# Optimization experiments

Hardware: AMD Instinct MI355X
Metric: run time of the kernel (lower is better)

## Reference

```python
import jax, jax.numpy as jnp
import numpy as np

HOP = 2
N = 16384
HIDDEN = 64


def setup_inputs() -> dict:
    key = jax.random.key(0)
    k1, k2, k3 = jax.random.split(key, 3)
    user_embs = jax.random.normal(k1, (N, HIDDEN), dtype=jnp.float32)
    adj = jax.random.uniform(k2, (N, N), dtype=jnp.float32)
    # xavier-uniform-like scale for [2*HIDDEN, HIDDEN] weights
    limit = float(np.sqrt(6.0 / (2 * HIDDEN + HIDDEN)))
    W = jax.random.uniform(k3, (HOP, 2 * HIDDEN, HIDDEN), dtype=jnp.float32,
                           minval=-limit, maxval=limit)
    return {"user_embs": user_embs, "adj": adj, "W": W}


def reference(user_embs, adj, W):
    # DiffNet social GCN: hop rounds of aggregate -> concat -> dense -> tanh.
    # Dropout omitted (eval mode, training=False).
    x = user_embs
    for k in range(HOP):
        agg = adj @ x                                  # [N, H] neighbor aggregation
        x = jnp.tanh(jnp.concatenate([agg, x], axis=1) @ W[k])  # [N, H]
    return x
```

## Files before the change

### kernel.cpp

```cpp
#include <hip/hip_runtime.h>
#include <hip/hip_bf16.h>
#include <math.h>

#define NROWS 16384
#define HID 64
#define KSPLIT 8
#define KCH (NROWS / KSPLIT)

typedef __attribute__((ext_vector_type(8))) __bf16 bf16x8;
typedef __attribute__((ext_vector_type(4))) float f32x4;

__device__ inline f32x4 mfma16(bf16x8 a, bf16x8 b, f32x4 c) {
    return __builtin_amdgcn_mfma_f32_16x16x32_bf16(a, b, c, 0, 0, 0);
}

__device__ inline void split8v(const f32x4 v0, const f32x4 v1, bf16x8& h, bf16x8& l) {
    float f[8] = {v0[0], v0[1], v0[2], v0[3], v1[0], v1[1], v1[2], v1[3]};
#pragma unroll
    for (int j = 0; j < 8; ++j) {
        __bf16 hh = (__bf16)f[j];
        h[j] = hh;
        l[j] = (__bf16)(f[j] - (float)hh);
    }
}

__global__ __launch_bounds__(256) void pack_b(const float* __restrict__ x,
                                              __bf16* __restrict__ hi,
                                              __bf16* __restrict__ lo) {
    __shared__ float tile[32 * 64];
    const int kb = blockIdx.x;
    const f32x4* src = (const f32x4*)(x + (size_t)kb * 32 * 64);
    f32x4* dst = (f32x4*)tile;
    dst[threadIdx.x] = src[threadIdx.x];
    dst[threadIdx.x + 256] = src[threadIdx.x + 256];
    __syncthreads();
    const int t = threadIdx.x >> 6;
    const int l = threadIdx.x & 63;
    const int col = (t << 4) + (l & 15);
    const int krow = (l >> 4) * 8;
    bf16x8 h8, l8;
#pragma unroll
    for (int j = 0; j < 8; ++j) {
        float v = tile[(krow + j) * 64 + col];
        __bf16 hh = (__bf16)v;
        h8[j] = hh;
        l8[j] = (__bf16)(v - (float)hh);
    }
    const size_t base = (((size_t)kb * 4 + t) * 64 + l) * 8;
    *(bf16x8*)(hi + base) = h8;
    *(bf16x8*)(lo + base) = l8;
}

__global__ __launch_bounds__(256, 2) void gemm_partial(const float* __restrict__ adj,
                                                       const __bf16* __restrict__ Bhi,
                                                       const __bf16* __restrict__ Blo,
                                                       float* __restrict__ partial) {
    const int lane = threadIdx.x & 63;
    const int wv = threadIdx.x >> 6;
    const int rt = blockIdx.x & 63;
    const int ks = blockIdx.x >> 6;
    const int rbase = rt * 256 + wv * 64;
    const int rq = lane & 15;
    const int kq = lane >> 4;

    f32x4 acc[4][4];
#pragma unroll
    for (int g = 0; g < 4; ++g)
#pragma unroll
        for (int t = 0; t < 4; ++t) acc[g][t] = f32x4{0.f, 0.f, 0.f, 0.f};

    const float* ap = adj + (size_t)(rbase + rq) * NROWS + ks * KCH + kq * 8;
    const int kk0 = ks * KCH;

    for (int kk = 0; kk < KCH; kk += 32) {
        f32x4 av[4][2];
#pragma unroll
        for (int g = 0; g < 4; ++g) {
            const f32x4* a = (const f32x4*)(ap + (size_t)(g * 16) * NROWS + kk);
            av[g][0] = a[0];
            av[g][1] = a[1];
        }
        const size_t bb = ((size_t)((kk0 + kk) >> 5) * 4) * 512 + (size_t)lane * 8;
        bf16x8 bh[4], bl[4];
#pragma unroll
        for (int t = 0; t < 4; ++t) {
            bh[t] = *(const bf16x8*)(Bhi + bb + (size_t)t * 512);
            bl[t] = *(const bf16x8*)(Blo + bb + (size_t)t * 512);
        }
#pragma unroll
        for (int g = 0; g < 4; ++g) {
            bf16x8 ah, al;
            split8v(av[g][0], av[g][1], ah, al);
#pragma unroll
            for (int t = 0; t < 4; ++t) {
                acc[g][t] = mfma16(ah, bh[t], acc[g][t]);
                acc[g][t] = mfma16(ah, bl[t], acc[g][t]);
                acc[g][t] = mfma16(al, bh[t], acc[g][t]);
            }
        }
    }

    float* pp = partial + (size_t)ks * (NROWS * HID) + (size_t)rbase * HID;
#pragma unroll
    for (int g = 0; g < 4; ++g)
#pragma unroll
        for (int t = 0; t < 4; ++t)
#pragma unroll
            for (int r = 0; r < 4; ++r)
                __builtin_nontemporal_store(acc[g][t][r],
                    pp + (g * 16 + kq * 4 + r) * HID + t * 16 + rq);
}

__global__ __launch_bounds__(256) void reduce_dense(const float* __restrict__ partial,
                                                    const float* __restrict__ xin,
                                                    const float* __restrict__ W,
                                                    float* __restrict__ xout) {
    __shared__ float wsm[128 * 64];
    const f32x4* wsrc = (const f32x4*)W;
    f32x4* wdst = (f32x4*)wsm;
#pragma unroll
    for (int i = 0; i < 8; ++i) wdst[threadIdx.x + 256 * i] = wsrc[threadIdx.x + 256 * i];
    __syncthreads();

    const int lane = threadIdx.x & 63;
    const int wv = threadIdx.x >> 6;
    const int r0 = blockIdx.x * 32 + wv * 8;
#pragma unroll 2
    for (int i = 0; i < 8; ++i) {
        const int r = r0 + i;
        float av = 0.f;
#pragma unroll
        for (int ks = 0; ks < KSPLIT; ++ks)
            av += partial[(size_t)ks * (NROWS * HID) + (size_t)r * HID + lane];
        const float xv = xin[(size_t)r * HID + lane];
        float z = 0.f;
#pragma unroll
        for (int j = 0; j < 64; ++j) z += __shfl(av, j) * wsm[j * 64 + lane];
#pragma unroll
        for (int j = 0; j < 64; ++j) z += __shfl(xv, j) * wsm[(64 + j) * 64 + lane];
        xout[(size_t)r * HID + lane] = tanhf(z);
    }
}

extern "C" void kernel_launch(void* const* d_in, const int* in_sizes, int n_in,
                              void* d_out, int out_size, void* d_ws, size_t ws_size,
                              hipStream_t stream) {
    const float* x0 = (const float*)d_in[0];
    const float* adj = (const float*)d_in[1];
    const float* W = (const float*)d_in[2];
    float* out = (float*)d_out;

    char* ws = (char*)d_ws;
    __bf16* Bhi = (__bf16*)(ws);
    __bf16* Blo = (__bf16*)(ws + (2u << 20));
    float* partial = (float*)(ws + (4u << 20));
    float* x1 = (float*)(ws + (36u << 20));

    pack_b<<<512, 256, 0, stream>>>(x0, Bhi, Blo);
    gemm_partial<<<KSPLIT * 64, 256, 0, stream>>>(adj, Bhi, Blo, partial);
    reduce_dense<<<512, 256, 0, stream>>>(partial, x0, W, x1);
    pack_b<<<512, 256, 0, stream>>>(x1, Bhi, Blo);
    gemm_partial<<<KSPLIT * 64, 256, 0, stream>>>(adj, Bhi, Blo, partial);
    reduce_dense<<<512, 256, 0, stream>>>(partial, x1, W + 128 * 64, out);
}
```

Before: 499.3 us.

## Stage packed B tiles through double-buffered shared memory in split-K GEMM

Instead of every wave loading the packed hi/lo bf16 B fragments directly from global memory, the block cooperatively loads one 64-k stage into registers, writes it to a double-buffered LDS tile, and all four waves read from LDS. The next stage's global load is issued before compute to overlap latency, and two 32-k sub-steps of A are loaded per stage. This cuts redundant global/L2 traffic for B by four, at the cost of 32KB LDS per block, a barrier per stage, and more registers for the doubled A prefetch, which may reduce occupancy.

```diff
diff --git a/kernel.cpp b/kernel.cpp
--- a/kernel.cpp
+++ b/kernel.cpp
@@ -6,6 +6,7 @@
 #define HID 64
 #define KSPLIT 8
 #define KCH (NROWS / KSPLIT)
+#define NSTAGE 32
 
 typedef __attribute__((ext_vector_type(8))) __bf16 bf16x8;
 typedef __attribute__((ext_vector_type(4))) float f32x4;
@@ -55,8 +56,11 @@
                                                        const __bf16* __restrict__ Bhi,
                                                        const __bf16* __restrict__ Blo,
                                                        float* __restrict__ partial) {
-    const int lane = threadIdx.x & 63;
-    const int wv = threadIdx.x >> 6;
+    __shared__ char bsm[2][16384];
+
+    const int tid = threadIdx.x;
+    const int lane = tid & 63;
+    const int wv = tid >> 6;
     const int rt = blockIdx.x & 63;
     const int ks = blockIdx.x >> 6;
     const int rbase = rt * 256 + wv * 64;
@@ -70,34 +74,73 @@
         for (int t = 0; t < 4; ++t) acc[g][t] = f32x4{0.f, 0.f, 0.f, 0.f};
 
     const float* ap = adj + (size_t)(rbase + rq) * NROWS + ks * KCH + kq * 8;
-    const int kk0 = ks * KCH;
-
-    for (int kk = 0; kk < KCH; kk += 32) {
-        f32x4 av[4][2];
-#pragma unroll
-        for (int g = 0; g < 4; ++g) {
-            const f32x4* a = (const f32x4*)(ap + (size_t)(g * 16) * NROWS + kk);
-            av[g][0] = a[0];
-            av[g][1] = a[1];
-        }
-        const size_t bb = ((size_t)((kk0 + kk) >> 5) * 4) * 512 + (size_t)lane * 8;
-        bf16x8 bh[4], bl[4];
-#pragma unroll
-        for (int t = 0; t < 4; ++t) {
-            bh[t] = *(const bf16x8*)(Bhi + bb + (size_t)t * 512);
-            bl[t] = *(const bf16x8*)(Blo + bb + (size_t)t * 512);
-        }
-#pragma unroll
-        for (int g = 0; g < 4; ++g) {
-            bf16x8 ah, al;
-            split8v(av[g][0], av[g][1], ah, al);
+    const __bf16* bhc = Bhi + (size_t)(ks * 64) * 2048;
+    const __bf16* blc = Blo + (size_t)(ks * 64) * 2048;
+
+    bf16x8 breg[4];
+#define LOADSTAGE(st)                                                          \
+    {                                                                          \
+        _Pragma("unroll") for (int j = 0; j < 4; ++j) {                        \
+            const int i = wv * 4 + j;                                          \
+            const __bf16* src = ((i >> 3) ? blc : bhc) +                       \
+                                (size_t)(2 * (st) + ((i >> 2) & 1)) * 2048 +   \
+                                (i & 3) * 512 + lane * 8;                      \
+            breg[j] = *(const bf16x8*)src;                                     \
+        }                                                                      \
+    }
+#define WRITESTAGE(buf)                                                        \
+    {                                                                          \
+        _Pragma("unroll") for (int j = 0; j < 4; ++j) {                        \
+            const int i = wv * 4 + j;                                          \
+            char* dst = bsm[buf] + (i >> 3) * 8192 + ((i >> 2) & 1) * 4096 +   \
+                        (i & 3) * 1024 + lane * 16;                            \
+            *(bf16x8*)dst = breg[j];                                           \
+        }                                                                      \
+    }
+
+    LOADSTAGE(0);
+    WRITESTAGE(0);
+    __syncthreads();
+
+    for (int st = 0; st < NSTAGE; ++st) {
+        const int buf = st & 1;
+        if (st + 1 < NSTAGE) LOADSTAGE(st + 1);
+
+        f32x4 av[2][4][2];
+#pragma unroll
+        for (int ss = 0; ss < 2; ++ss)
+#pragma unroll
+            for (int g = 0; g < 4; ++g) {
+                const f32x4* a = (const f32x4*)(ap + (size_t)(g * 16) * NROWS +
+                                                (2 * st + ss) * 32);
+                av[ss][g][0] = a[0];
+                av[ss][g][1] = a[1];
+            }
+
+#pragma unroll
+        for (int ss = 0; ss < 2; ++ss) {
+            const char* hib = bsm[buf] + ss * 4096 + lane * 16;
+            bf16x8 bh[4], bl[4];
 #pragma unroll
             for (int t = 0; t < 4; ++t) {
-                acc[g][t] = mfma16(ah, bh[t], acc[g][t]);
-                acc[g][t] = mfma16(ah, bl[t], acc[g][t]);
-                acc[g][t] = mfma16(al, bh[t], acc[g][t]);
+                bh[t] = *(const bf16x8*)(hib + t * 1024);
+                bl[t] = *(const bf16x8*)(hib + 8192 + t * 1024);
+            }
+#pragma unroll
+            for (int g = 0; g < 4; ++g) {
+                bf16x8 ah, al;
+                split8v(av[ss][g][0], av[ss][g][1], ah, al);
+#pragma unroll
+                for (int t = 0; t < 4; ++t) {
+                    acc[g][t] = mfma16(ah, bh[t], acc[g][t]);
+                    acc[g][t] = mfma16(ah, bl[t], acc[g][t]);
+                    acc[g][t] = mfma16(al, bh[t], acc[g][t]);
+                }
             }
         }
+
+        if (st + 1 < NSTAGE) WRITESTAGE(buf ^ 1);
+        __syncthreads();
     }
 
     float* pp = partial + (size_t)ks * (NROWS * HID) + (size_t)rbase * HID;
```

Result: slower. 511.8 us (+2.5%).

## Double rows per wave in GEMM and fuse bf16 packing into reduce kernel

Applied to the files above, without the earlier changes.

Each wave of the split-K GEMM now computes 128 rows with two register-held A groups. This halves the grid to one block per CU and doubles reuse of the loaded B fragments. The reduce_dense kernel optionally writes the hi/lo bf16 packed form of its output, which removes the separate pack_b launch between hops. The cost is higher register pressure and lower occupancy, which may reduce memory latency hiding on the adj stream.

```diff
diff --git a/kernel.cpp b/kernel.cpp
--- a/kernel.cpp
+++ b/kernel.cpp
@@ -51,21 +51,21 @@
     *(bf16x8*)(lo + base) = l8;
 }
 
-__global__ __launch_bounds__(256, 2) void gemm_partial(const float* __restrict__ adj,
+__global__ __launch_bounds__(256, 1) void gemm_partial(const float* __restrict__ adj,
                                                        const __bf16* __restrict__ Bhi,
                                                        const __bf16* __restrict__ Blo,
                                                        float* __restrict__ partial) {
     const int lane = threadIdx.x & 63;
     const int wv = threadIdx.x >> 6;
-    const int rt = blockIdx.x & 63;
-    const int ks = blockIdx.x >> 6;
-    const int rbase = rt * 256 + wv * 64;
+    const int rt = blockIdx.x & 31;
+    const int ks = blockIdx.x >> 5;
+    const int rbase = rt * 512 + wv * 128;
     const int rq = lane & 15;
     const int kq = lane >> 4;
 
-    f32x4 acc[4][4];
-#pragma unroll
-    for (int g = 0; g < 4; ++g)
+    f32x4 acc[8][4];
+#pragma unroll
+    for (int g = 0; g < 8; ++g)
 #pragma unroll
         for (int t = 0; t < 4; ++t) acc[g][t] = f32x4{0.f, 0.f, 0.f, 0.f};
 
@@ -73,12 +73,12 @@
     const int kk0 = ks * KCH;
 
     for (int kk = 0; kk < KCH; kk += 32) {
-        f32x4 av[4][2];
+        f32x4 av0[4][2];
 #pragma unroll
         for (int g = 0; g < 4; ++g) {
             const f32x4* a = (const f32x4*)(ap + (size_t)(g * 16) * NROWS + kk);
-            av[g][0] = a[0];
-            av[g][1] = a[1];
+            av0[g][0] = a[0];
+            av0[g][1] = a[1];
         }
         const size_t bb = ((size_t)((kk0 + kk) >> 5) * 4) * 512 + (size_t)lane * 8;
         bf16x8 bh[4], bl[4];
@@ -87,10 +87,17 @@
             bh[t] = *(const bf16x8*)(Bhi + bb + (size_t)t * 512);
             bl[t] = *(const bf16x8*)(Blo + bb + (size_t)t * 512);
         }
+        f32x4 av1[4][2];
+#pragma unroll
+        for (int g = 0; g < 4; ++g) {
+            const f32x4* a = (const f32x4*)(ap + (size_t)((g + 4) * 16) * NROWS + kk);
+            av1[g][0] = a[0];
+            av1[g][1] = a[1];
+        }
 #pragma unroll
         for (int g = 0; g < 4; ++g) {
             bf16x8 ah, al;
-            split8v(av[g][0], av[g][1], ah, al);
+            split8v(av0[g][0], av0[g][1], ah, al);
 #pragma unroll
             for (int t = 0; t < 4; ++t) {
                 acc[g][t] = mfma16(ah, bh[t], acc[g][t]);
@@ -98,11 +105,22 @@
                 acc[g][t] = mfma16(al, bh[t], acc[g][t]);
             }
         }
+#pragma unroll
+        for (int g = 0; g < 4; ++g) {
+            bf16x8 ah, al;
+            split8v(av1[g][0], av1[g][1], ah, al);
+#pragma unroll
+            for (int t = 0; t < 4; ++t) {
+                acc[g + 4][t] = mfma16(ah, bh[t], acc[g + 4][t]);
+                acc[g + 4][t] = mfma16(ah, bl[t], acc[g + 4][t]);
+                acc[g + 4][t] = mfma16(al, bh[t], acc[g + 4][t]);
+            }
+        }
     }
 
     float* pp = partial + (size_t)ks * (NROWS * HID) + (size_t)rbase * HID;
 #pragma unroll
-    for (int g = 0; g < 4; ++g)
+    for (int g = 0; g < 8; ++g)
 #pragma unroll
         for (int t = 0; t < 4; ++t)
 #pragma unroll
@@ -114,8 +132,11 @@
 __global__ __launch_bounds__(256) void reduce_dense(const float* __restrict__ partial,
                                                     const float* __restrict__ xin,
                                                     const float* __restrict__ W,
-                                                    float* __restrict__ xout) {
+                                                    float* __restrict__ xout,
+                                                    __bf16* __restrict__ hi,
+                                                    __bf16* __restrict__ lo) {
     __shared__ float wsm[128 * 64];
+    __shared__ float xt[32][64];
     const f32x4* wsrc = (const f32x4*)W;
     f32x4* wdst = (f32x4*)wsm;
 #pragma unroll
@@ -138,7 +159,28 @@
         for (int j = 0; j < 64; ++j) z += __shfl(av, j) * wsm[j * 64 + lane];
 #pragma unroll
         for (int j = 0; j < 64; ++j) z += __shfl(xv, j) * wsm[(64 + j) * 64 + lane];
-        xout[(size_t)r * HID + lane] = tanhf(z);
+        const float v = tanhf(z);
+        xout[(size_t)r * HID + lane] = v;
+        xt[wv * 8 + i][lane] = v;
+    }
+
+    if (hi != nullptr) {
+        __syncthreads();
+        const int t = threadIdx.x >> 6;
+        const int l = threadIdx.x & 63;
+        const int col = (t << 4) + (l & 15);
+        const int krow = (l >> 4) * 8;
+        bf16x8 h8, l8;
+#pragma unroll
+        for (int j = 0; j < 8; ++j) {
+            float v = xt[krow + j][col];
+            __bf16 hh = (__bf16)v;
+            h8[j] = hh;
+            l8[j] = (__bf16)(v - (float)hh);
+        }
+        const size_t base = (((size_t)blockIdx.x * 4 + t) * 64 + l) * 8;
+        *(bf16x8*)(hi + base) = h8;
+        *(bf16x8*)(lo + base) = l8;
     }
 }
 
@@ -157,9 +199,8 @@
     float* x1 = (float*)(ws + (36u << 20));
 
     pack_b<<<512, 256, 0, stream>>>(x0, Bhi, Blo);
-    gemm_partial<<<KSPLIT * 64, 256, 0, stream>>>(adj, Bhi, Blo, partial);
-    reduce_dense<<<512, 256, 0, stream>>>(partial, x0, W, x1);
-    pack_b<<<512, 256, 0, stream>>>(x1, Bhi, Blo);
-    gemm_partial<<<KSPLIT * 64, 256, 0, stream>>>(adj, Bhi, Blo, partial);
-    reduce_dense<<<512, 256, 0, stream>>>(partial, x1, W + 128 * 64, out);
-}
+    gemm_partial<<<KSPLIT * 32, 256, 0, stream>>>(adj, Bhi, Blo, partial);
+    reduce_dense<<<512, 256, 0, stream>>>(partial, x0, W, x1, Bhi, Blo);
+    gemm_partial<<<KSPLIT * 32, 256, 0, stream>>>(adj, Bhi, Blo, partial);
+    reduce_dense<<<512, 256, 0, stream>>>(partial, x1, W + 128 * 64, out, nullptr, nullptr);
+}
```

Result: faster. 453.8 us (median of 2 runs) (-9.1%).
